# Kernel optimization log

Measured on AMD Instinct MI355X. Metric: run time of the kernel, lower is better.

## Reference

```python
import jax, jax.numpy as jnp
import numpy as np
import math

HS_MIN = 1e-07
MASK_BOUND = 5e-08


def setup_inputs() -> dict:
    key = jax.random.key(0)
    N, B, D = 256, 128, 784
    k0, k1, k2 = jax.random.split(key, 3)
    bandwidth = (4.0 * np.sqrt(math.pi) / (math.pi ** 4 * N)) ** 0.2
    return {
        "x": jax.random.normal(k0, (B, D), jnp.float32),
        "log_det": jnp.zeros((B,), jnp.float32),
        "datapoints": jax.random.normal(k1, (N, D), jnp.float32),
        "log_hs": jnp.full((N, D), np.log(bandwidth), jnp.float32),
        "kde_weights": jnp.zeros((N, D), jnp.float32),
        "vs": jax.random.normal(k2, (D, D), jnp.float32),
    }


def _householder(vs):
    # Q = prod_i (I - 2 v_i v_i^T), applied as rank-1 updates via scan.
    D = vs.shape[1]
    def step(Q, v):
        vn = v / jnp.linalg.norm(v)
        return Q - 2.0 * jnp.outer(Q @ vn, vn), None
    Q, _ = jax.lax.scan(step, jnp.eye(D, dtype=vs.dtype), vs)
    return Q


def _kde_logs(x, datapoints, log_hs, kde_weights):
    # Shared [N,B,D] diff/softplus term feeding log_cdf, log_sf, log_pdf.
    hs = jnp.maximum(jnp.exp(log_hs), HS_MIN)
    log_hs_c = jnp.maximum(log_hs, math.log(HS_MIN))
    u = -(x[None, ...] - datapoints[:, None, :]) / hs[:, None, :]  # [N,B,D]
    w = (kde_weights - jax.nn.logsumexp(kde_weights, axis=0, keepdims=True))[:, None, :]
    sp = jax.nn.softplus(u)
    log_cdf = jax.nn.logsumexp(-sp + w, axis=0)                          # [B,D]
    log_sf = jax.nn.logsumexp(u - sp + w, axis=0)                        # [B,D]
    log_pdf = jax.nn.logsumexp(u - log_hs_c[:, None, :] - 2.0 * sp + w, axis=0)
    return log_cdf, log_sf, log_pdf


def reference(x, log_det, datapoints, log_hs, kde_weights, vs):
    log_cdf_l, log_sf_l, log_pdf = _kde_logs(x, datapoints, log_hs, kde_weights)
    cdf_l = jnp.exp(log_cdf_l)

    cdf_mask = ((cdf_l > MASK_BOUND) & (cdf_l < 1.0 - MASK_BOUND)).astype(x.dtype)
    cdf_l_good = cdf_l * cdf_mask + 0.5 * (1.0 - cdf_mask)
    inverse_l = jax.scipy.special.ndtri(cdf_l_good)

    cdf_mask_right = (cdf_l >= 1.0 - MASK_BOUND).astype(x.dtype)
    cdf_l_bad_right_log = log_sf_l * cdf_mask_right + (-1.0) * (1.0 - cdf_mask_right)
    inverse_l = inverse_l + jnp.sqrt(-2.0 * cdf_l_bad_right_log) * cdf_mask_right

    cdf_mask_left = (cdf_l <= MASK_BOUND).astype(x.dtype)
    cdf_l_bad_left_log = log_cdf_l * cdf_mask_left + (-1.0) * (1.0 - cdf_mask_left)
    inverse_l = inverse_l - jnp.sqrt(-2.0 * cdf_l_bad_left_log) * cdf_mask_left

    log_norm = -0.5 * inverse_l ** 2 - 0.5 * math.log(2.0 * math.pi)
    log_gauss_deriv = (
        log_norm * cdf_mask
        + (jnp.log(jnp.sqrt(-2.0 * cdf_l_bad_left_log)) - log_cdf_l) * cdf_mask_left
        + (jnp.log(jnp.sqrt(-2.0 * cdf_l_bad_right_log)) - log_sf_l) * cdf_mask_right
    )
    log_det = log_det + jnp.sum(log_pdf - log_gauss_deriv, axis=-1)

    Q = _householder(vs)
    x_out = inverse_l @ Q
    return x_out, log_det
```

## Files before the change

kernel.cpp:

```cpp
#include <hip/hip_runtime.h>
#include <math.h>

#define NP 256
#define BB 128
#define DD 784
#define HS_MIN 1e-7f
#define LOG_HS_MIN -16.11809565095832f
#define LOG_MB -16.811242831518264f
#define NEG_HALF_LOG_2PI -0.9189385332046727f
#define W 8
#define NW 98

__device__ double ndtri_logs(float log_cdf_f, float log_sf_f) {
    double lp = (double)log_cdf_f;
    double ls = (double)log_sf_f;
    double p = (double)__expf(log_cdf_f);
    double q = p - 0.5;
    if (fabs(q) <= 0.425) {
        double r = 0.180625 - q * q;
        double num = (((((((2.5090809287301226727e3 * r + 3.3430575583588128105e4) * r
                         + 6.7265770927008700853e4) * r + 4.5921953931549871457e4) * r
                         + 1.3731693765509461125e4) * r + 1.9715909503065514427e3) * r
                         + 1.3314166789178437745e2) * r + 3.3871328727963666080e0);
        double den = (((((((5.2264952788528545610e3 * r + 2.8729085735721942674e4) * r
                         + 3.9307895800092710610e4) * r + 2.1213794301586595867e4) * r
                         + 5.3941960214247511077e3) * r + 6.8718700749205790830e2) * r
                         + 4.2313330701600911252e1) * r + 1.0);
        return q * num / den;
    }
    double r = (q < 0.0) ? sqrt(-lp) : sqrt(-ls);
    double v;
    if (r <= 5.0) {
        r -= 1.6;
        double num = (((((((7.74545014278341407640e-4 * r + 2.27238449892691845833e-2) * r
                         + 2.41780725177450611770e-1) * r + 1.27045825245236838258e0) * r
                         + 3.64784832476320460504e0) * r + 5.76949722146069140550e0) * r
                         + 4.63033784615654529590e0) * r + 1.42343711074968357734e0);
        double den = (((((((1.05075007164441684324e-9 * r + 5.47593808499534494600e-4) * r
                         + 1.51986665636164571966e-2) * r + 1.48103976427480074590e-1) * r
                         + 6.89767334985100004550e-1) * r + 1.67638483018380384940e0) * r
                         + 2.05319162663775882187e0) * r + 1.0);
        v = num / den;
    } else {
        r -= 5.0;
        double num = (((((((2.01033439929228813265e-7 * r + 2.71155556874348757815e-5) * r
                         + 1.24266094738807843860e-3) * r + 2.65321895265761230930e-2) * r
                         + 2.96560571828504891230e-1) * r + 1.78482653991729133580e0) * r
                         + 5.46378491116411436990e0) * r + 6.65790464350110377720e0);
        double den = (((((((2.04426310338993978564e-15 * r + 1.42151175831644588870e-7) * r
                         + 1.84631831751005468180e-5) * r + 7.86869131145613259100e-4) * r
                         + 1.48753612908506148525e-2) * r + 1.36929880922735805310e-1) * r
                         + 5.99832206555887937690e-1) * r + 1.0);
        v = num / den;
    }
    return (q < 0.0) ? -v : v;
}

__global__ __launch_bounds__(256) void k_lseprep(const float* __restrict__ kw,
                                                 const float* __restrict__ log_hs,
                                                 const float* __restrict__ dp,
                                                 float4* __restrict__ pk) {
    __shared__ float red[4];
    int d = blockIdx.x;
    int n = threadIdx.x;
    float a = kw[n * DD + d];
    float m = a;
    #pragma unroll
    for (int off = 32; off; off >>= 1) m = fmaxf(m, __shfl_xor(m, off, 64));
    if ((threadIdx.x & 63) == 0) red[threadIdx.x >> 6] = m;
    __syncthreads();
    m = fmaxf(fmaxf(red[0], red[1]), fmaxf(red[2], red[3]));
    __syncthreads();
    float e = __expf(a - m);
    #pragma unroll
    for (int off = 32; off; off >>= 1) e += __shfl_xor(e, off, 64);
    if ((threadIdx.x & 63) == 0) red[threadIdx.x >> 6] = e;
    __syncthreads();
    float lse = m + __logf(red[0] + red[1] + red[2] + red[3]);

    int idx = n * DD + d;
    float lh = log_hs[idx];
    float hs = fmaxf(__expf(lh), HS_MIN);
    float lhc = fmaxf(lh, LOG_HS_MIN);
    float wv = kw[idx] - lse;
    pk[idx] = make_float4(dp[idx], 1.f / hs, __expf(wv), __expf(wv - lhc));
}

__global__ __launch_bounds__(256) void k_vngram(const float* __restrict__ vs,
                                                float* __restrict__ VN,
                                                float* __restrict__ G) {
    __shared__ float L[W * DD];
    __shared__ float red[4];
    __shared__ float nrm[W];
    int wi = blockIdx.x;
    int t = threadIdx.x;
    const float* src = vs + (size_t)wi * (W * DD);
    for (int j = t; j < W * DD; j += 256) L[j] = src[j];
    __syncthreads();

    for (int r = 0; r < W; ++r) {
        float ss = 0.f;
        for (int j = t; j < DD; j += 256) {
            float v = L[r * DD + j];
            ss += v * v;
        }
        #pragma unroll
        for (int off = 32; off; off >>= 1) ss += __shfl_down(ss, off, 64);
        if ((t & 63) == 0) red[t >> 6] = ss;
        __syncthreads();
        if (t == 0) nrm[r] = rsqrtf(red[0] + red[1] + red[2] + red[3]);
        __syncthreads();
    }

    for (int j = t; j < W * DD; j += 256) {
        int r = j / DD;
        float v = L[j] * nrm[r];
        L[j] = v;
        VN[(size_t)wi * (W * DD) + j] = v;
    }
    __syncthreads();

    if (t < 64) {
        int k = t >> 3, i = t & 7;
        const float4* a = (const float4*)(L + k * DD);
        const float4* b = (const float4*)(L + i * DD);
        float s = 0.f;
        for (int j = 0; j < DD / 4; ++j) {
            float4 av = a[j], bv = b[j];
            s += av.x * bv.x + av.y * bv.y + av.z * bv.z + av.w * bv.w;
        }
        G[wi * 64 + k * 8 + i] = s;
    }
}

__global__ __launch_bounds__(256) void k_main(const float* __restrict__ x,
                                              const float4* __restrict__ pk,
                                              float* __restrict__ Y,
                                              float* __restrict__ T) {
    unsigned t = blockIdx.x * 256u + threadIdx.x;
    unsigned b = t / DD;
    unsigned d = t - b * DD;
    float xv = x[t];
    float s1 = 0.f, s2 = 0.f, s3 = 0.f;
    for (int n = 0; n < NP; ++n) {
        float4 c = pk[n * DD + d];
        float u = (c.x - xv) * c.y;
        float e = __expf(-fabsf(u));
        float r = 1.f / (1.f + e);
        float base = c.z * r;
        float eh = (u >= 0.f) ? e : 1.f;
        float el = (u >= 0.f) ? 1.f : e;
        s1 += base * eh;
        s2 += base * el;
        s3 += c.w * (e * r * r);
    }
    float log_cdf = __logf(s1);
    float log_sf  = __logf(s2);
    float log_pdf = __logf(s3);

    bool right = (log_sf  <= LOG_MB);
    bool left  = (log_cdf <= LOG_MB);

    float inv, lgd;
    if (right) {
        float t2 = -2.f * log_sf;
        inv = sqrtf(t2);
        lgd = 0.5f * __logf(t2) - log_sf;
    } else if (left) {
        float t2 = -2.f * log_cdf;
        inv = -sqrtf(t2);
        lgd = 0.5f * __logf(t2) - log_cdf;
    } else {
        inv = (float)ndtri_logs(log_cdf, log_sf);
        lgd = -0.5f * inv * inv + NEG_HALF_LOG_2PI;
    }
    Y[t] = inv;
    T[t] = log_pdf - lgd;
}

__device__ __forceinline__ float wave_red_sum(float x) {
    x += __int_as_float(__builtin_amdgcn_update_dpp(0, __float_as_int(x), 0x111, 0xf, 0xf, true));
    x += __int_as_float(__builtin_amdgcn_update_dpp(0, __float_as_int(x), 0x112, 0xf, 0xf, true));
    x += __int_as_float(__builtin_amdgcn_update_dpp(0, __float_as_int(x), 0x114, 0xf, 0xf, true));
    x += __int_as_float(__builtin_amdgcn_update_dpp(0, __float_as_int(x), 0x118, 0xf, 0xf, true));
    x += __int_as_float(__builtin_amdgcn_update_dpp(0, __float_as_int(x), 0x142, 0xa, 0xf, true));
    x += __int_as_float(__builtin_amdgcn_update_dpp(0, __float_as_int(x), 0x143, 0xc, 0xf, true));
    return __int_as_float(__builtin_amdgcn_readlane(__float_as_int(x), 63));
}

__global__ __launch_bounds__(64, 1) void k_house(const float* __restrict__ Yin,
                                                 const float* __restrict__ T,
                                                 const float* __restrict__ ld_in,
                                                 const float* __restrict__ VN,
                                                 const float* __restrict__ G,
                                                 float* __restrict__ out) {
    __shared__ float gld[NW * 64];
    const int b = blockIdx.x;
    const int l = threadIdx.x;
    const int toff = 768 + (l & 15);
    const bool thas = (l < 16);

    {
        float s = 0.f;
        #pragma unroll
        for (int i = 0; i < 12; ++i) s += T[b * DD + 64 * i + l];
        if (thas) s += T[b * DD + 768 + l];
        float tot = wave_red_sum(s);
        if (l == 0) out[BB * DD + b] = ld_in[b] + tot;
    }

    for (int i = l; i < NW * 64; i += 64) gld[i] = G[i];
    __syncthreads();

    float4 y[3];
    float ytl;
    #pragma unroll
    for (int i = 0; i < 3; ++i)
        y[i] = *(const float4*)(Yin + b * DD + 256 * i + 4 * l);
    ytl = thas ? Yin[b * DD + toff] : 0.f;

    for (int wi = 0; wi < NW; ++wi) {
        const float* Vw = VN + (size_t)wi * (W * DD);
        const float* Gw = gld + wi * 64;

        float4 v[W][3];
        float vt[W];
        #pragma unroll
        for (int r = 0; r < W; ++r) {
            const float* vr = Vw + r * DD;
            #pragma unroll
            for (int i = 0; i < 3; ++i)
                v[r][i] = *(const float4*)(vr + 256 * i + 4 * l);
            vt[r] = thas ? vr[toff] : 0.f;
        }

        float p[W];
        #pragma unroll
        for (int r = 0; r < W; ++r) {
            float s = 0.f;
            #pragma unroll
            for (int i = 0; i < 3; ++i) {
                s += y[i].x * v[r][i].x + y[i].y * v[r][i].y
                   + y[i].z * v[r][i].z + y[i].w * v[r][i].w;
            }
            s += ytl * vt[r];
            p[r] = wave_red_sum(s);
        }

        float sv[W];
        #pragma unroll
        for (int r = 0; r < W; ++r) {
            float acc = p[r];
            #pragma unroll
            for (int k = 0; k < W; ++k)
                if (k < r) acc -= 2.f * Gw[k * 8 + r] * sv[k];
            sv[r] = acc;
        }

        #pragma unroll
        for (int r = 0; r < W; ++r) {
            float c = 2.f * sv[r];
            #pragma unroll
            for (int i = 0; i < 3; ++i) {
                y[i].x -= c * v[r][i].x;  y[i].y -= c * v[r][i].y;
                y[i].z -= c * v[r][i].z;  y[i].w -= c * v[r][i].w;
            }
            ytl -= c * vt[r];
        }
    }

    #pragma unroll
    for (int i = 0; i < 3; ++i)
        *(float4*)(out + b * DD + 256 * i + 4 * l) = y[i];
    if (thas)
        out[b * DD + toff] = ytl;
}

extern "C" void kernel_launch(void* const* d_in, const int* in_sizes, int n_in,
                              void* d_out, int out_size, void* d_ws, size_t ws_size,
                              hipStream_t stream) {
    const float* x      = (const float*)d_in[0];
    const float* ld_in  = (const float*)d_in[1];
    const float* dp     = (const float*)d_in[2];
    const float* log_hs = (const float*)d_in[3];
    const float* kw     = (const float*)d_in[4];
    const float* vs     = (const float*)d_in[5];
    float* out = (float*)d_out;

    float* ws   = (float*)d_ws;
    float4* pk  = (float4*)(ws + 1024);
    float* Y    = ws + 1024 + NP * DD * 4;
    float* T    = Y + BB * DD;
    float* VN   = T + BB * DD;
    float* G    = VN + DD * DD;

    k_lseprep<<<DD, 256, 0, stream>>>(kw, log_hs, dp, pk);
    k_vngram<<<NW, 256, 0, stream>>>(vs, VN, G);
    k_main<<<(BB * DD) / 256, 256, 0, stream>>>(x, pk, Y, T);
    k_house<<<BB, 64, 0, stream>>>(Y, T, ld_in, VN, G, out);
}
```

Measured before the change: 247.8 us.

## Fuse KDE parameter prep into main KDE kernel using shared-memory staging

Merges the per-dimension weight normalization kernel with the main KDE accumulation kernel. Each block handles one dimension d, builds the 256 packed datapoint parameters in shared memory, and then 128 threads (one per batch row) loop over them. This removes the global pk buffer round-trip and one launch. In exchange, only half of each block's threads do the heavy loop, the grid is 784 blocks, and x reads and Y/T writes become strided by DD, so they are uncoalesced.

```diff
diff --git a/kernel.cpp b/kernel.cpp
--- a/kernel.cpp
+++ b/kernel.cpp
@@ -56,34 +56,81 @@
     return (q < 0.0) ? -v : v;
 }
 
-__global__ __launch_bounds__(256) void k_lseprep(const float* __restrict__ kw,
-                                                 const float* __restrict__ log_hs,
-                                                 const float* __restrict__ dp,
-                                                 float4* __restrict__ pk) {
+__global__ __launch_bounds__(256) void k_kde(const float* __restrict__ kw,
+                                             const float* __restrict__ log_hs,
+                                             const float* __restrict__ dp,
+                                             const float* __restrict__ x,
+                                             float* __restrict__ Y,
+                                             float* __restrict__ T) {
     __shared__ float red[4];
+    __shared__ float4 pkL[NP];
     int d = blockIdx.x;
     int n = threadIdx.x;
+
     float a = kw[n * DD + d];
     float m = a;
     #pragma unroll
     for (int off = 32; off; off >>= 1) m = fmaxf(m, __shfl_xor(m, off, 64));
-    if ((threadIdx.x & 63) == 0) red[threadIdx.x >> 6] = m;
+    if ((n & 63) == 0) red[n >> 6] = m;
     __syncthreads();
     m = fmaxf(fmaxf(red[0], red[1]), fmaxf(red[2], red[3]));
     __syncthreads();
     float e = __expf(a - m);
     #pragma unroll
     for (int off = 32; off; off >>= 1) e += __shfl_xor(e, off, 64);
-    if ((threadIdx.x & 63) == 0) red[threadIdx.x >> 6] = e;
+    if ((n & 63) == 0) red[n >> 6] = e;
     __syncthreads();
     float lse = m + __logf(red[0] + red[1] + red[2] + red[3]);
 
-    int idx = n * DD + d;
-    float lh = log_hs[idx];
-    float hs = fmaxf(__expf(lh), HS_MIN);
-    float lhc = fmaxf(lh, LOG_HS_MIN);
-    float wv = kw[idx] - lse;
-    pk[idx] = make_float4(dp[idx], 1.f / hs, __expf(wv), __expf(wv - lhc));
+    {
+        int idx = n * DD + d;
+        float lh = log_hs[idx];
+        float hs = fmaxf(__expf(lh), HS_MIN);
+        float lhc = fmaxf(lh, LOG_HS_MIN);
+        float wv = a - lse;
+        pkL[n] = make_float4(dp[idx], 1.f / hs, __expf(wv), __expf(wv - lhc));
+    }
+    __syncthreads();
+
+    if (n < BB) {
+        int b = n;
+        float xv = x[b * DD + d];
+        float s1 = 0.f, s2 = 0.f, s3 = 0.f;
+        for (int k = 0; k < NP; ++k) {
+            float4 c = pkL[k];
+            float u = (c.x - xv) * c.y;
+            float ee = __expf(-fabsf(u));
+            float r = 1.f / (1.f + ee);
+            float base = c.z * r;
+            float eh = (u >= 0.f) ? ee : 1.f;
+            float el = (u >= 0.f) ? 1.f : ee;
+            s1 += base * eh;
+            s2 += base * el;
+            s3 += c.w * (ee * r * r);
+        }
+        float log_cdf = __logf(s1);
+        float log_sf  = __logf(s2);
+        float log_pdf = __logf(s3);
+
+        bool right = (log_sf  <= LOG_MB);
+        bool left  = (log_cdf <= LOG_MB);
+
+        float inv, lgd;
+        if (right) {
+            float t2 = -2.f * log_sf;
+            inv = sqrtf(t2);
+            lgd = 0.5f * __logf(t2) - log_sf;
+        } else if (left) {
+            float t2 = -2.f * log_cdf;
+            inv = -sqrtf(t2);
+            lgd = 0.5f * __logf(t2) - log_cdf;
+        } else {
+            inv = (float)ndtri_logs(log_cdf, log_sf);
+            lgd = -0.5f * inv * inv + NEG_HALF_LOG_2PI;
+        }
+        Y[b * DD + d] = inv;
+        T[b * DD + d] = log_pdf - lgd;
+    }
 }
 
 __global__ __launch_bounds__(256) void k_vngram(const float* __restrict__ vs,
@@ -131,51 +178,6 @@
         }
         G[wi * 64 + k * 8 + i] = s;
     }
-}
-
-__global__ __launch_bounds__(256) void k_main(const float* __restrict__ x,
-                                              const float4* __restrict__ pk,
-                                              float* __restrict__ Y,
-                                              float* __restrict__ T) {
-    unsigned t = blockIdx.x * 256u + threadIdx.x;
-    unsigned b = t / DD;
-    unsigned d = t - b * DD;
-    float xv = x[t];
-    float s1 = 0.f, s2 = 0.f, s3 = 0.f;
-    for (int n = 0; n < NP; ++n) {
-        float4 c = pk[n * DD + d];
-        float u = (c.x - xv) * c.y;
-        float e = __expf(-fabsf(u));
-        float r = 1.f / (1.f + e);
-        float base = c.z * r;
-        float eh = (u >= 0.f) ? e : 1.f;
-        float el = (u >= 0.f) ? 1.f : e;
-        s1 += base * eh;
-        s2 += base * el;
-        s3 += c.w * (e * r * r);
-    }
-    float log_cdf = __logf(s1);
-    float log_sf  = __logf(s2);
-    float log_pdf = __logf(s3);
-
-    bool right = (log_sf  <= LOG_MB);
-    bool left  = (log_cdf <= LOG_MB);
-
-    float inv, lgd;
-    if (right) {
-        float t2 = -2.f * log_sf;
-        inv = sqrtf(t2);
-        lgd = 0.5f * __logf(t2) - log_sf;
-    } else if (left) {
-        float t2 = -2.f * log_cdf;
-        inv = -sqrtf(t2);
-        lgd = 0.5f * __logf(t2) - log_cdf;
-    } else {
-        inv = (float)ndtri_logs(log_cdf, log_sf);
-        lgd = -0.5f * inv * inv + NEG_HALF_LOG_2PI;
-    }
-    Y[t] = inv;
-    T[t] = log_pdf - lgd;
 }
 
 __device__ __forceinline__ float wave_red_sum(float x) {
@@ -288,14 +290,12 @@
     float* out = (float*)d_out;
 
     float* ws   = (float*)d_ws;
-    float4* pk  = (float4*)(ws + 1024);
-    float* Y    = ws + 1024 + NP * DD * 4;
+    float* Y    = ws + 1024;
     float* T    = Y + BB * DD;
     float* VN   = T + BB * DD;
     float* G    = VN + DD * DD;
 
-    k_lseprep<<<DD, 256, 0, stream>>>(kw, log_hs, dp, pk);
     k_vngram<<<NW, 256, 0, stream>>>(vs, VN, G);
-    k_main<<<(BB * DD) / 256, 256, 0, stream>>>(x, pk, Y, T);
+    k_kde<<<DD, 256, 0, stream>>>(kw, log_hs, dp, x, Y, T);
     k_house<<<BB, 64, 0, stream>>>(Y, T, ld_in, VN, G, out);
 }
```

Result: faster. 235.3 us (-5.1%).
